# Optimization experiments

Measured on AMD Instinct MI355X. Metric: run time of the kernel, lower is better.

Reference implementation:

```python
import jax, jax.numpy as jnp
import numpy as np

G, M, H, HEADS, FFN, MAX_DIST, E = 8, 1024, 256, 8, 1024, 5, 131072
N = G * M
HD = H // HEADS

def _ln(x, g, b, eps=1e-5):
    m = x.mean(-1, keepdims=True)
    v = ((x - m) ** 2).mean(-1, keepdims=True)
    return (x - m) / jnp.sqrt(v + eps) * g + b

def _forward(x, gcn_w, gcn_b, qkv_w, qkv_b, proj_w, proj_b,
             ln1_g, ln1_b, ln2_g, ln2_b, ffn1_w, ffn1_b, ffn2_w, ffn2_b,
             bias_emb, oln1_g, oln1_b, oln2_g, oln2_b,
             offn1_w, offn1_b, offn2_w, offn2_b, edge_index, batch):
    src, dst = edge_index[0], edge_index[1]
    # --- local conv: GCNConv (self-loops + symmetric normalization) ---
    sl = jnp.arange(N, dtype=src.dtype)
    s2 = jnp.concatenate([src, sl]); d2 = jnp.concatenate([dst, sl])
    xw = x @ gcn_w.T
    deg = jax.ops.segment_sum(jnp.ones_like(d2, dtype=x.dtype), d2, num_segments=N)
    dinv = jnp.where(deg > 0, 1.0 / jnp.sqrt(deg), 0.0)
    norm = dinv[s2] * dinv[d2]
    x_local = jax.ops.segment_sum(xw[s2] * norm[:, None], d2, num_segments=N) + gcn_b
    # --- to_dense_batch ---
    counts = jax.ops.segment_sum(jnp.ones(N, jnp.int32), batch, num_segments=G)
    starts = jnp.concatenate([jnp.zeros(1, jnp.int32), jnp.cumsum(counts)[:-1]])
    local = jnp.arange(N, dtype=jnp.int32) - starts[batch]
    dense_x = jnp.zeros((G, M, H), x.dtype).at[batch, local].set(x)
    mask = jnp.zeros((G, M), bool).at[batch, local].set(True)
    # --- SPD via batched boolean adjacency powering (== per-node BFS capped at MAX_DIST) ---
    g_e = batch[src]
    valid = (batch[src] == batch[dst]) & (src != dst)
    ls, ld = local[src], local[dst]
    adj = jnp.zeros((G, M, M), bool).at[g_e, ls, ld].max(valid).at[g_e, ld, ls].max(valid)
    dist = jnp.full((G, M, M), MAX_DIST + 1, jnp.int32)
    eye = jnp.eye(M, dtype=bool)[None]
    dist = jnp.where(eye & mask[:, :, None], 0, dist)
    reach = adj
    dist = jnp.where(reach, jnp.minimum(dist, 1), dist)
    for d in range(2, MAX_DIST + 1):
        reach = jnp.einsum('gij,gjk->gik', reach.astype(x.dtype), adj.astype(x.dtype)) > 0
        dist = jnp.where(reach, jnp.minimum(dist, d), dist)
    attn_bias = bias_emb[dist][..., 0]  # [G, M, M]
    # --- Graphormer encoder layer (layers=1) ---
    h = dense_x
    qkv = (h @ qkv_w.T + qkv_b).reshape(G, M, 3, HEADS, HD).transpose(2, 0, 3, 1, 4)
    q, k, v = qkv[0], qkv[1], qkv[2]  # [G, heads, M, hd]
    scores = jnp.einsum('ghqd,ghkd->ghqk', q, k) * (HD ** -0.5)
    scores = scores + attn_bias[:, None].astype(scores.dtype)
    pad = ~mask
    scores = jnp.where(pad[:, None, None, :], -jnp.inf, scores)
    attn = jax.nn.softmax(scores, axis=-1)
    out = jnp.einsum('ghqk,ghkd->ghqd', attn, v).transpose(0, 2, 1, 3).reshape(G, M, H)
    out = out @ proj_w.T + proj_b
    h = _ln(h + out, ln1_g, ln1_b)
    ff = jax.nn.gelu(h @ ffn1_w.T + ffn1_b, approximate=False) @ ffn2_w.T + ffn2_b
    h = _ln(h + ff, ln2_g, ln2_b)
    h = jnp.where(pad[..., None], 0.0, h)
    x_global = h[batch, local]
    # --- GPS combine + outer FFN (dropout = identity at eval) ---
    y = _ln(x + (x_local + x_global), oln1_g, oln1_b)
    ff2 = jax.nn.gelu(y @ offn1_w.T + offn1_b, approximate=False) @ offn2_w.T + offn2_b
    return _ln(y + ff2, oln2_g, oln2_b)

def setup_inputs() -> dict:
    key = jax.random.key(0)
    ks = jax.random.split(key, 16)
    w = lambda k, *s: jax.random.normal(k, s, jnp.float32) * 0.02
    src = jax.random.randint(ks[0], (E,), 0, N, jnp.int32)
    # keep each edge inside one graph (graphs are contiguous blocks of M nodes)
    dst = (src // M) * M + jax.random.randint(ks[1], (E,), 0, M, jnp.int32)
    return dict(
        x=jax.random.normal(ks[2], (N, H), jnp.float32),
        gcn_w=w(ks[3], H, H), gcn_b=jnp.zeros((H,), jnp.float32),
        qkv_w=w(ks[4], 3 * H, H), qkv_b=jnp.zeros((3 * H,), jnp.float32),
        proj_w=w(ks[5], H, H), proj_b=jnp.zeros((H,), jnp.float32),
        ln1_g=jnp.ones((H,), jnp.float32), ln1_b=jnp.zeros((H,), jnp.float32),
        ln2_g=jnp.ones((H,), jnp.float32), ln2_b=jnp.zeros((H,), jnp.float32),
        ffn1_w=w(ks[6], FFN, H), ffn1_b=jnp.zeros((FFN,), jnp.float32),
        ffn2_w=w(ks[7], H, FFN), ffn2_b=jnp.zeros((H,), jnp.float32),
        bias_emb=w(ks[8], MAX_DIST + 2, 1),
        oln1_g=jnp.ones((H,), jnp.float32), oln1_b=jnp.zeros((H,), jnp.float32),
        oln2_g=jnp.ones((H,), jnp.float32), oln2_b=jnp.zeros((H,), jnp.float32),
        offn1_w=w(ks[9], FFN, H), offn1_b=jnp.zeros((FFN,), jnp.float32),
        offn2_w=w(ks[10], H, FFN), offn2_b=jnp.zeros((H,), jnp.float32),
        edge_index=jnp.stack([src, dst]),
        batch=(jnp.arange(N, dtype=jnp.int32) // M),
    )

def reference(x, gcn_w, gcn_b, qkv_w, qkv_b, proj_w, proj_b,
              ln1_g, ln1_b, ln2_g, ln2_b, ffn1_w, ffn1_b, ffn2_w, ffn2_b,
              bias_emb, oln1_g, oln1_b, oln2_g, oln2_b,
              offn1_w, offn1_b, offn2_w, offn2_b, edge_index, batch):
    return _forward(x, gcn_w, gcn_b, qkv_w, qkv_b, proj_w, proj_b,
                    ln1_g, ln1_b, ln2_g, ln2_b, ffn1_w, ffn1_b, ffn2_w, ffn2_b,
                    bias_emb, oln1_g, oln1_b, oln2_g, oln2_b,
                    offn1_w, offn1_b, offn2_w, offn2_b, edge_index, batch)
```

## Files before the change

### kernel.cpp

```cpp
#include <hip/hip_runtime.h>
#include <hip/hip_bf16.h>
#include <cstdint>

#define G 8
#define M 1024
#define H 256
#define HEADS 8
#define FFND 1024
#define NE 131072
#define NN (G*M)
#define HD 32

typedef unsigned long long u64;
typedef uint8_t u8;
typedef unsigned short ushort_t;
typedef __attribute__((ext_vector_type(8))) short bf16x8;
typedef __attribute__((ext_vector_type(4))) float f32x4;

__device__ __forceinline__ short f2b(float v) {
  __hip_bfloat16 h = __float2bfloat16(v);
  return *reinterpret_cast<short*>(&h);
}
__device__ __forceinline__ float b2f(unsigned int u) {
  union { float f; unsigned int i; } v; v.i = u << 16; return v.f;
}

typedef __attribute__((address_space(1))) const void gvoid;
typedef __attribute__((address_space(3))) void lvoid;
__device__ __forceinline__ void gload16(const void* g, void* l) {
  __builtin_amdgcn_global_load_lds((gvoid*)g, (lvoid*)l, 16, 0, 0);
}

__global__ void k_prep(const int* __restrict__ srcv, const int* __restrict__ dstv,
                       int* __restrict__ deg, int* __restrict__ deg2) {
  int e = blockIdx.x * 256 + threadIdx.x;
  if (e >= NE) return;
  int d = dstv[e], s = srcv[e];
  atomicAdd(&deg[d], 1);
  if (s != d) { atomicAdd(&deg2[s], 1); atomicAdd(&deg2[d], 1); }
}

__global__ __launch_bounds__(1024) void k_scan2(const int* __restrict__ deg, const int* __restrict__ deg2,
                                                int* __restrict__ starts, int* __restrict__ starts2,
                                                float* __restrict__ dinv) {
  __shared__ int tmp[1024];
  const int* in = blockIdx.x ? deg2 : deg;
  int* outp = blockIdx.x ? starts2 : starts;
  int t = threadIdx.x;
  int base = t * 8;
  int v[8]; int s = 0;
  #pragma unroll
  for (int i = 0; i < 8; ++i) { v[i] = in[base + i]; s += v[i]; }
  if (blockIdx.x == 0) {
    #pragma unroll
    for (int i = 0; i < 8; ++i) dinv[base + i] = rsqrtf((float)(v[i] + 1));
  }
  tmp[t] = s;
  __syncthreads();
  for (int off = 1; off < 1024; off <<= 1) {
    int x = (t >= off) ? tmp[t - off] : 0;
    __syncthreads();
    tmp[t] += x;
    __syncthreads();
  }
  int ex = (t == 0) ? 0 : tmp[t - 1];
  #pragma unroll
  for (int i = 0; i < 8; ++i) { outp[base + i] = ex; ex += v[i]; }
}

__global__ void k_fillb(const int* __restrict__ srcv, const int* __restrict__ dstv,
                        const int* __restrict__ starts, int* __restrict__ cursor,
                        int* __restrict__ csr,
                        const int* __restrict__ starts2, int* __restrict__ cur2,
                        int* __restrict__ nbr) {
  int e = blockIdx.x * 256 + threadIdx.x;
  if (e >= NE) return;
  int d = dstv[e], s = srcv[e];
  int pos = atomicAdd(&cursor[d], 1);
  csr[starts[d] + pos] = s;
  if (s != d) {
    int p = atomicAdd(&cur2[s], 1); nbr[starts2[s] + p] = d;
    p = atomicAdd(&cur2[d], 1);     nbr[starts2[d] + p] = s;
  }
}

__global__ __launch_bounds__(256) void k_gather(const int* __restrict__ csr,
    const int* __restrict__ starts, const int* __restrict__ deg,
    const float* __restrict__ dinv, const ushort_t* __restrict__ xwb,
    const float* __restrict__ gcn_b, float* __restrict__ xloc) {
  int d = blockIdx.x, t = threadIdx.x;
  int s0 = starts[d], cnt = deg[d];
  float acc = 0.f;
  for (int j = 0; j < cnt; ++j) {
    int s = csr[s0 + j];
    acc += dinv[s] * b2f(xwb[(size_t)s * H + t]);
  }
  float di = dinv[d];
  float self = b2f(xwb[(size_t)d * H + t]);
  xloc[(size_t)d * H + t] = di * acc + di * di * self + gcn_b[t];
}

__global__ __launch_bounds__(1024) void k_spdm(const int* __restrict__ starts2,
                                               const int* __restrict__ deg2,
                                               const int* __restrict__ nbr,
                                               u8* __restrict__ dist) {
  __shared__ unsigned int Abuf[1024], Bbuf[1024];
  __shared__ u8 dtile[1024][32];
  const int g = blockIdx.x >> 5, w = blockIdx.x & 31;
  const int i = threadIdx.x;
  const int gi = (g << 10) | i;
  unsigned int self = ((i >> 5) == w) ? (1u << (i & 31)) : 0u;
  Abuf[i] = self;
  uint4 six; six.x = six.y = six.z = six.w = 0x06060606u;
  *reinterpret_cast<uint4*>(&dtile[i][0])  = six;
  *reinterpret_cast<uint4*>(&dtile[i][16]) = six;
  if (self) dtile[i][i & 31] = 0;
  const int s0 = starts2[gi], cnt = deg2[gi];
  unsigned int* prev = Abuf;
  unsigned int* cur  = Bbuf;
  unsigned int vis = self;
  __syncthreads();
  for (int l = 1; l <= 5; ++l) {
    unsigned int acc = vis;
    for (int e = 0; e < cnt; ++e)
      acc |= prev[nbr[s0 + e] & 1023];
    unsigned int newly = acc & ~vis;
    while (newly) {
      int k = __ffs(newly) - 1;
      newly &= newly - 1;
      dtile[i][k] = (u8)l;
    }
    cur[i] = acc;
    vis = acc;
    __syncthreads();
    unsigned int* tsw = prev; prev = cur; cur = tsw;
  }
  u8* drow = dist + ((size_t)gi << 10) + w * 32;
  *reinterpret_cast<uint4*>(drow)      = *reinterpret_cast<const uint4*>(&dtile[i][0]);
  *reinterpret_cast<uint4*>(drow + 16) = *reinterpret_cast<const uint4*>(&dtile[i][16]);
}

#define WB_GCN   0
#define WB_QKV   65536
#define WB_PROJ  262144
#define WB_FFN1  327680
#define WB_FFN2  589824
#define WB_OFFN1 851968
#define WB_OFFN2 1114112
#define WB_TOTAL 1376256
#define NXBLK 2048
#define NWBLK 5376

__global__ void k_cvtall(const float* __restrict__ x,
                         const float* p0, const float* p1, const float* p2,
                         const float* p3, const float* p4, const float* p5, const float* p6,
                         const float* __restrict__ qkv_b,
                         ushort_t* __restrict__ x_bf, ushort_t* __restrict__ w_bf,
                         float* __restrict__ bias_cat) {
  int bid = blockIdx.x, t = threadIdx.x;
  if (bid < NXBLK) {
    int i = bid * 256 + t;
    float4 v = reinterpret_cast<const float4*>(x)[i];
    unsigned int lo = (unsigned int)(ushort_t)f2b(v.x) | ((unsigned int)(ushort_t)f2b(v.y) << 16);
    unsigned int hi = (unsigned int)(ushort_t)f2b(v.z) | ((unsigned int)(ushort_t)f2b(v.w) << 16);
    reinterpret_cast<uint2*>(x_bf)[i] = make_uint2(lo, hi);
  } else if (bid < NXBLK + NWBLK) {
    int i = (bid - NXBLK) * 256 + t;
    const float* src; int off;
    if (i < WB_QKV)        { src = p0; off = i; }
    else if (i < WB_PROJ)  { src = p1; off = i - WB_QKV; }
    else if (i < WB_FFN1)  { src = p2; off = i - WB_PROJ; }
    else if (i < WB_FFN2)  { src = p3; off = i - WB_FFN1; }
    else if (i < WB_OFFN1) { src = p4; off = i - WB_FFN2; }
    else if (i < WB_OFFN2) { src = p5; off = i - WB_OFFN1; }
    else                   { src = p6; off = i - WB_OFFN2; }
    w_bf[i] = (ushort_t)f2b(src[off]);
  } else {
    for (int i = t; i < 1024; i += 256) bias_cat[i] = (i < 256) ? 0.f : qkv_b[i - 256];
  }
}

template<int BM, int ACT, int OMODE>
__global__ __launch_bounds__(256) void k_mgemm(const short* __restrict__ A,
                                               const short* __restrict__ W,
                                               const float* __restrict__ bias,
                                               short* __restrict__ Cb,
                                               short* __restrict__ Cb2,
                                               int K, int O) {
  constexpr int FM = BM / 32;
  __shared__ __attribute__((aligned(16))) short As[BM * 64];
  __shared__ __attribute__((aligned(16))) short Ws[64 * 64];
  const int tid = threadIdx.x;
  const int lane = tid & 63, wbase = tid & 192;
  const int wid = tid >> 6;
  const int lg = lane >> 4, lr = lane & 15;
  const int wm = wid >> 1, wn = wid & 1;
  const int m0 = blockIdx.y * BM, n0 = blockIdx.x * 64;
  f32x4 acc[FM][2];
  #pragma unroll
  for (int i = 0; i < FM; ++i)
    #pragma unroll
    for (int j = 0; j < 2; ++j)
      acc[i][j] = (f32x4){0.f, 0.f, 0.f, 0.f};

  for (int k0 = 0; k0 < K; k0 += 64) {
    #pragma unroll
    for (int c = 0; c < BM / 32; ++c) {
      int chunk = c * 256 + tid;
      int row = chunk >> 3, ks = chunk & 7;
      int srcks = ks ^ (row & 7);
      gload16(A + (size_t)(m0 + row) * K + k0 + srcks * 8,
              (char*)As + (c * 256 + wbase) * 16);
    }
    #pragma unroll
    for (int c = 0; c < 2; ++c) {
      int chunk = c * 256 + tid;
      int row = chunk >> 3, ks = chunk & 7;
      int srcks = ks ^ (row & 7);
      gload16(W + (size_t)(n0 + row) * K + k0 + srcks * 8,
              (char*)Ws + (c * 256 + wbase) * 16);
    }
    __syncthreads();
    #pragma unroll
    for (int kk = 0; kk < 2; ++kk) {
      const int d = kk * 4 + lg;
      bf16x8 b[2];
      #pragma unroll
      for (int fn = 0; fn < 2; ++fn) {
        int r = wn * 32 + fn * 16 + lr;
        b[fn] = *reinterpret_cast<const bf16x8*>((const char*)Ws + r * 128 + ((d ^ (r & 7)) * 16));
      }
      #pragma unroll
      for (int fm = 0; fm < FM; ++fm) {
        int r = wm * (BM / 2) + fm * 16 + lr;
        bf16x8 a = *reinterpret_cast<const bf16x8*>((const char*)As + r * 128 + ((d ^ (r & 7)) * 16));
        acc[fm][0] = __builtin_amdgcn_mfma_f32_16x16x32_bf16(a, b[0], acc[fm][0], 0, 0, 0);
        acc[fm][1] = __builtin_amdgcn_mfma_f32_16x16x32_bf16(a, b[1], acc[fm][1], 0, 0, 0);
      }
    }
    __syncthreads();
  }
  #pragma unroll
  for (int fm = 0; fm < FM; ++fm)
    #pragma unroll
    for (int fn = 0; fn < 2; ++fn)
      #pragma unroll
      for (int rg = 0; rg < 4; ++rg) {
        int r = m0 + wm * (BM / 2) + fm * 16 + lg * 4 + rg;
        int cc = n0 + wn * 32 + fn * 16 + lr;
        float v = acc[fm][fn][rg] + (bias ? bias[cc] : 0.f);
        if (ACT == 1) v = 0.5f * v * (1.0f + erff(v * 0.70710678118654752f));
        if (OMODE == 1) Cb[(size_t)r * O + cc] = f2b(v);
        else {
          if (cc < 256) Cb2[(size_t)r * 256 + cc] = f2b(v);
          else          Cb[(size_t)r * 768 + cc - 256] = f2b(v);
        }
      }
}

template<int KK, int OUTB>
__global__ __launch_bounds__(256) void k_gemmln(const short* __restrict__ A,
                                                const short* __restrict__ W,
                                                const float* __restrict__ bias,
                                                const float* __restrict__ res1,
                                                const float* __restrict__ gam,
                                                const float* __restrict__ bet,
                                                float* __restrict__ outf,
                                                ushort_t* __restrict__ outb) {
  __shared__ __attribute__((aligned(16))) short As[32 * 64];
  __shared__ __attribute__((aligned(16))) short Ws[256 * 64];
  __shared__ float redS[4][32], redQ[4][32];
  const int tid = threadIdx.x, lane = tid & 63, wid = tid >> 6;
  const int wbase = tid & 192;
  const int lg = lane >> 4, lr = lane & 15;
  const int m0 = blockIdx.x * 32;
  f32x4 acc[2][4];
  #pragma unroll
  for (int i = 0; i < 2; ++i)
    #pragma unroll
    for (int j = 0; j < 4; ++j)
      acc[i][j] = (f32x4){0.f, 0.f, 0.f, 0.f};

  for (int k0 = 0; k0 < KK; k0 += 64) {
    {
      int row = tid >> 3, ks = tid & 7, srcks = ks ^ (row & 7);
      gload16(A + (size_t)(m0 + row) * KK + k0 + srcks * 8,
              (char*)As + wbase * 16);
    }
    #pragma unroll
    for (int c = 0; c < 8; ++c) {
      int chunk = c * 256 + tid;
      int row = chunk >> 3, ks = chunk & 7;
      int srcks = ks ^ (row & 7);
      gload16(W + (size_t)row * KK + k0 + srcks * 8,
              (char*)Ws + (c * 256 + wbase) * 16);
    }
    __syncthreads();
    #pragma unroll
    for (int kk = 0; kk < 2; ++kk) {
      const int d = kk * 4 + lg;
      bf16x8 a[2];
      #pragma unroll
      for (int fr = 0; fr < 2; ++fr) {
        int r = fr * 16 + lr;
        a[fr] = *reinterpret_cast<const bf16x8*>((const char*)As + r * 128 + ((d ^ (r & 7)) * 16));
      }
      #pragma unroll
      for (int fc = 0; fc < 4; ++fc) {
        int r = wid * 64 + fc * 16 + lr;
        bf16x8 b = *reinterpret_cast<const bf16x8*>((const char*)Ws + r * 128 + ((d ^ (r & 7)) * 16));
        acc[0][fc] = __builtin_amdgcn_mfma_f32_16x16x32_bf16(a[0], b, acc[0][fc], 0, 0, 0);
        acc[1][fc] = __builtin_amdgcn_mfma_f32_16x16x32_bf16(a[1], b, acc[1][fc], 0, 0, 0);
      }
    }
    __syncthreads();
  }

  float vs[2][4][4];
  float ps[2][4], pq[2][4];
  #pragma unroll
  for (int fr = 0; fr < 2; ++fr)
    #pragma unroll
    for (int rg = 0; rg < 4; ++rg) { ps[fr][rg] = 0.f; pq[fr][rg] = 0.f; }
  #pragma unroll
  for (int fc = 0; fc < 4; ++fc) {
    int col = wid * 64 + fc * 16 + lr;
    float bv = bias[col];
    #pragma unroll
    for (int fr = 0; fr < 2; ++fr)
      #pragma unroll
      for (int rg = 0; rg < 4; ++rg) {
        int row = m0 + fr * 16 + 4 * lg + rg;
        float v = acc[fr][fc][rg] + bv + res1[(size_t)row * 256 + col];
        vs[fr][fc][rg] = v;
        ps[fr][rg] += v; pq[fr][rg] += v * v;
      }
  }
  #pragma unroll
  for (int fr = 0; fr < 2; ++fr)
    #pragma unroll
    for (int rg = 0; rg < 4; ++rg) {
      float s = ps[fr][rg], q = pq[fr][rg];
      s += __shfl_xor(s, 1); q += __shfl_xor(q, 1);
      s += __shfl_xor(s, 2); q += __shfl_xor(q, 2);
      s += __shfl_xor(s, 4); q += __shfl_xor(q, 4);
      s += __shfl_xor(s, 8); q += __shfl_xor(q, 8);
      ps[fr][rg] = s; pq[fr][rg] = q;
    }
  if (lr == 0) {
    #pragma unroll
    for (int fr = 0; fr < 2; ++fr)
      #pragma unroll
      for (int rg = 0; rg < 4; ++rg) {
        redS[wid][fr * 16 + 4 * lg + rg] = ps[fr][rg];
        redQ[wid][fr * 16 + 4 * lg + rg] = pq[fr][rg];
      }
  }
  __syncthreads();
  #pragma unroll
  for (int fr = 0; fr < 2; ++fr)
    #pragma unroll
    for (int rg = 0; rg < 4; ++rg) {
      int rl = fr * 16 + 4 * lg + rg;
      float S = redS[0][rl] + redS[1][rl] + redS[2][rl] + redS[3][rl];
      float Q = redQ[0][rl] + redQ[1][rl] + redQ[2][rl] + redQ[3][rl];
      float mean = S * (1.0f / 256.0f);
      float rstd = rsqrtf(Q * (1.0f / 256.0f) - mean * mean + 1e-5f);
      #pragma unroll
      for (int fc = 0; fc < 4; ++fc) {
        int col = wid * 64 + fc * 16 + lr;
        float v = (vs[fr][fc][rg] - mean) * rstd * gam[col] + bet[col];
        size_t o = (size_t)(m0 + rl) * 256 + col;
        outf[o] = v;
        if (OUTB) outb[o] = (ushort_t)f2b(v);
      }
    }
}

__global__ __launch_bounds__(256) void k_attn(const ushort_t* __restrict__ qkv,
                                              const u8* __restrict__ dist,
                                              const float* __restrict__ emb,
                                              short* __restrict__ attno) {
  __shared__ __attribute__((aligned(16))) char KsB[32 * 128];
  __shared__ __attribute__((aligned(16))) char VtB[32 * 128 + 64];
  __shared__ __attribute__((aligned(16))) char PB[4][16 * 128];
  __shared__ __attribute__((aligned(16))) u8 Ds[32 * 128];
  __shared__ float semb[8];
  const int g = blockIdx.z, head = blockIdx.y;
  const int q0 = blockIdx.x * 64;
  const int t = threadIdx.x, lane = t & 63, wid = t >> 6;
  const int lg = lane >> 4, lr = lane & 15;
  if (t < 7) semb[t] = emb[t] * 1.44269504088896341f;
  const size_t nodebase = (size_t)(g * M) * 768;
  const float C1 = 0.17677669529663687f * 1.44269504088896341f;

  bf16x8 qfrag = *reinterpret_cast<const bf16x8*>(
      qkv + nodebase + (size_t)(q0 + wid * 16 + lr) * 768 + head * 32 + lg * 8);

  const int srow = t >> 2, sc = t & 3;
  const int prow8 = t >> 3, pslot = (t & 7) ^ (prow8 & 7);
  uint4 kr, vr, dr;
  {
    size_t kn = nodebase + (size_t)(srow) * 768 + head * 32;
    kr = *reinterpret_cast<const uint4*>(qkv + kn + 256 + sc * 8);
    vr = *reinterpret_cast<const uint4*>(qkv + kn + 512 + sc * 8);
    dr = *reinterpret_cast<const uint4*>(dist + (size_t)(g * M + srow) * M + q0 + sc * 16);
  }

  f32x4 o0 = {0.f, 0.f, 0.f, 0.f}, o1 = {0.f, 0.f, 0.f, 0.f};
  float lpart[4] = {0.f, 0.f, 0.f, 0.f};
  char* pb = PB[wid];
  const int kp = srow >> 1;
  const int odd = srow & 1;
  const int d0 = sc * 8;
  int r8f[4], slK[4], slD[4];
  #pragma unroll
  for (int fn = 0; fn < 4; ++fn) {
    r8f[fn] = fn * 8 + (lr >> 1);
    slK[fn] = (((lr & 1) << 2) | lg) ^ (r8f[fn] & 7);
    slD[fn] = (((lr & 1) << 2) | wid) ^ (r8f[fn] & 7);
  }

  for (int kt = 0; kt < 16; ++kt) {
    *reinterpret_cast<uint4*>(KsB + prow8 * 128 + pslot * 16) = kr;
    *reinterpret_cast<uint4*>(Ds + prow8 * 128 + pslot * 16) = dr;
    {
      uint4 pvr;
      pvr.x = (unsigned int)__shfl_xor((int)vr.x, 4);
      pvr.y = (unsigned int)__shfl_xor((int)vr.y, 4);
      pvr.z = (unsigned int)__shfl_xor((int)vr.z, 4);
      pvr.w = (unsigned int)__shfl_xor((int)vr.w, 4);
      unsigned int ev[4], ov[4];
      ev[0] = odd ? pvr.x : vr.x; ev[1] = odd ? pvr.y : vr.y;
      ev[2] = odd ? pvr.z : vr.z; ev[3] = odd ? pvr.w : vr.w;
      ov[0] = odd ? vr.x : pvr.x; ov[1] = odd ? vr.y : pvr.y;
      ov[2] = odd ? vr.z : pvr.z; ov[3] = odd ? vr.w : pvr.w;
      #pragma unroll
      for (int di = 0; di < 4; ++di) {
        int dd = odd * 4 + di;
        int d = d0 + dd;
        unsigned int e16 = (dd & 1) ? (ev[dd >> 1] >> 16) : (ev[dd >> 1] & 0xffff);
        unsigned int o16 = (dd & 1) ? (ov[dd >> 1] >> 16) : (ov[dd >> 1] & 0xffff);
        *reinterpret_cast<unsigned int*>(VtB + d * 128 + ((d >> 3) << 4) + ((kp << 2) ^ ((d & 7) << 4)))
            = e16 | (o16 << 16);
      }
    }
    __syncthreads();

    {
      int ktn = (kt + 1) & 15;
      size_t kn = nodebase + (size_t)(ktn * 64 + srow) * 768 + head * 32;
      kr = *reinterpret_cast<const uint4*>(qkv + kn + 256 + sc * 8);
      vr = *reinterpret_cast<const uint4*>(qkv + kn + 512 + sc * 8);
      dr = *reinterpret_cast<const uint4*>(dist + (size_t)(g * M + ktn * 64 + srow) * M + q0 + sc * 16);
    }

    f32x4 s[4];
    unsigned int d4[4];
    #pragma unroll
    for (int fn = 0; fn < 4; ++fn) {
      bf16x8 b = *reinterpret_cast<const bf16x8*>(KsB + r8f[fn] * 128 + slK[fn] * 16);
      s[fn] = __builtin_amdgcn_mfma_f32_16x16x32_bf16(qfrag, b, (f32x4){0.f,0.f,0.f,0.f}, 0, 0, 0);
      d4[fn] = *reinterpret_cast<const unsigned int*>(Ds + r8f[fn] * 128 + slD[fn] * 16 + 4 * lg);
    }
    #pragma unroll
    for (int fn = 0; fn < 4; ++fn)
      #pragma unroll
      for (int rg = 0; rg < 4; ++rg)
        s[fn][rg] = exp2f(s[fn][rg] * C1 + semb[(d4[fn] >> (8 * rg)) & 255]);
    #pragma unroll
    for (int rg = 0; rg < 4; ++rg)
      lpart[rg] += (s[0][rg] + s[1][rg]) + (s[2][rg] + s[3][rg]);

    #pragma unroll
    for (int fn = 0; fn < 4; ++fn)
      #pragma unroll
      for (int rg = 0; rg < 4; ++rg) {
        int qq = 4 * lg + rg, key = fn * 16 + lr;
        *reinterpret_cast<ushort_t*>(pb + qq * 128 + ((key * 2) ^ ((qq & 7) << 4))) =
            (ushort_t)f2b(s[fn][rg]);
      }

    #pragma unroll
    for (int kh = 0; kh < 2; ++kh) {
      int c = kh * 4 + lg;
      int chx = (c << 4) ^ ((lr & 7) << 4);
      bf16x8 a  = *reinterpret_cast<const bf16x8*>(pb + lr * 128 + chx);
      bf16x8 b0 = *reinterpret_cast<const bf16x8*>(VtB + lr * 128 + ((lr >> 3) << 4) + chx);
      bf16x8 b1 = *reinterpret_cast<const bf16x8*>(VtB + (16 + lr) * 128 + (((16 + lr) >> 3) << 4) + chx);
      o0 = __builtin_amdgcn_mfma_f32_16x16x32_bf16(a, b0, o0, 0, 0, 0);
      o1 = __builtin_amdgcn_mfma_f32_16x16x32_bf16(a, b1, o1, 0, 0, 0);
    }
    __syncthreads();
  }

  #pragma unroll
  for (int rg = 0; rg < 4; ++rg) {
    float l = lpart[rg];
    l += __shfl_xor(l, 1);
    l += __shfl_xor(l, 2);
    l += __shfl_xor(l, 4);
    l += __shfl_xor(l, 8);
    float inv = 1.0f / l;
    size_t qn = (size_t)(g * M + q0 + wid * 16 + 4 * lg + rg);
    attno[qn * H + head * 32 + lr]      = f2b(o0[rg] * inv);
    attno[qn * H + head * 32 + 16 + lr] = f2b(o1[rg] * inv);
  }
}

__global__ __launch_bounds__(256) void k_ln(const float* __restrict__ a, const float* __restrict__ b,
                                            const float* __restrict__ c3,
                                            const float* __restrict__ gam, const float* __restrict__ bet,
                                            float* __restrict__ out, ushort_t* __restrict__ outb) {
  int wid = threadIdx.x >> 6, lane = threadIdx.x & 63;
  int row = blockIdx.x * 4 + wid;
  size_t base = (size_t)row * H + lane * 4;
  float4 v = *reinterpret_cast<const float4*>(a + base);
  float4 vb = *reinterpret_cast<const float4*>(b + base);
  v.x += vb.x; v.y += vb.y; v.z += vb.z; v.w += vb.w;
  if (c3) {
    float4 vc = *reinterpret_cast<const float4*>(c3 + base);
    v.x += vc.x; v.y += vc.y; v.z += vc.z; v.w += vc.w;
  }
  float s = v.x + v.y + v.z + v.w;
  float s2 = v.x*v.x + v.y*v.y + v.z*v.z + v.w*v.w;
  #pragma unroll
  for (int off = 1; off <= 32; off <<= 1) {
    s  += __shfl_xor(s, off);
    s2 += __shfl_xor(s2, off);
  }
  float mean = s * (1.0f / 256.0f);
  float rstd = rsqrtf(s2 * (1.0f / 256.0f) - mean * mean + 1e-5f);
  float4 gg = *reinterpret_cast<const float4*>(gam + lane * 4);
  float4 bb = *reinterpret_cast<const float4*>(bet + lane * 4);
  float4 r;
  r.x = (v.x - mean) * rstd * gg.x + bb.x;
  r.y = (v.y - mean) * rstd * gg.y + bb.y;
  r.z = (v.z - mean) * rstd * gg.z + bb.z;
  r.w = (v.w - mean) * rstd * gg.w + bb.w;
  *reinterpret_cast<float4*>(out + base) = r;
  if (outb) {
    unsigned int lo = (unsigned int)(ushort_t)f2b(r.x) | ((unsigned int)(ushort_t)f2b(r.y) << 16);
    unsigned int hi = (unsigned int)(ushort_t)f2b(r.z) | ((unsigned int)(ushort_t)f2b(r.w) << 16);
    *reinterpret_cast<uint2*>(outb + base) = make_uint2(lo, hi);
  }
}

extern "C" void kernel_launch(void* const* d_in, const int* in_sizes, int n_in,
                              void* d_out, int out_size, void* d_ws, size_t ws_size,
                              hipStream_t stream) {
  const float* x      = (const float*)d_in[0];
  const float* gcn_w  = (const float*)d_in[1];
  const float* gcn_b  = (const float*)d_in[2];
  const float* qkv_w  = (const float*)d_in[3];
  const float* qkv_b  = (const float*)d_in[4];
  const float* proj_w = (const float*)d_in[5];
  const float* proj_b = (const float*)d_in[6];
  const float* ln1_g  = (const float*)d_in[7];
  const float* ln1_b  = (const float*)d_in[8];
  const float* ln2_g  = (const float*)d_in[9];
  const float* ln2_b  = (const float*)d_in[10];
  const float* ffn1_w = (const float*)d_in[11];
  const float* ffn1_b = (const float*)d_in[12];
  const float* ffn2_w = (const float*)d_in[13];
  const float* ffn2_b = (const float*)d_in[14];
  const float* bias_e = (const float*)d_in[15];
  const float* oln1_g = (const float*)d_in[16];
  const float* oln1_b = (const float*)d_in[17];
  const float* oln2_g = (const float*)d_in[18];
  const float* oln2_b = (const float*)d_in[19];
  const float* offn1_w= (const float*)d_in[20];
  const float* offn1_b= (const float*)d_in[21];
  const float* offn2_w= (const float*)d_in[22];
  const float* offn2_b= (const float*)d_in[23];
  const int*   eidx   = (const int*)d_in[24];
  const int* esrc = eidx;
  const int* edst = eidx + NE;

  char* wsp = (char*)d_ws;
  size_t off = 0;
  auto alloc = [&](size_t bytes) { void* p = wsp + off; off += (bytes + 255) & ~255ull; return p; };
  const size_t SZ_NH = (size_t)NN * H * 4;
  ushort_t* x_bf  = (ushort_t*)alloc((size_t)NN * H * 2);
  ushort_t* w_bf  = (ushort_t*)alloc((size_t)WB_TOTAL * 2);
  float* bias_cat = (float*)alloc(1024 * 4);
  ushort_t* xwb   = (ushort_t*)alloc((size_t)NN * H * 2);
  float* xloc = (float*)alloc(SZ_NH);
  float* dinv = (float*)alloc((size_t)NN * 4);
  int*   deg  = (int*)  alloc((size_t)NN * 4);
  int* cursor = (int*)  alloc((size_t)NN * 4);
  int*  deg2  = (int*)  alloc((size_t)NN * 4);
  int* cursor2= (int*)  alloc((size_t)NN * 4);
  int* starts = (int*)  alloc((size_t)NN * 4);
  int* starts2= (int*)  alloc((size_t)NN * 4);
  int*   csr  = (int*)  alloc((size_t)NE * 4);
  int*   nbr  = (int*)  alloc((size_t)2 * NE * 4);
  u8*    dist = (u8*)   alloc((size_t)NN * M);
  ushort_t* qkvb = (ushort_t*)alloc((size_t)NN * 768 * 2);
  float* h1   = (float*)alloc(SZ_NH);
  ushort_t* h1_bf = (ushort_t*)alloc((size_t)NN * H * 2);
  float* h2   = (float*)alloc(SZ_NH);
  float* y    = (float*)alloc(SZ_NH);

  ushort_t* attno = x_bf;
  ushort_t* mid = (ushort_t*)dist;
  ushort_t* y_bf = h1_bf;
  float* outp = (float*)d_out;

  ushort_t* proj_wb = w_bf + WB_PROJ;
  ushort_t* ffn1_wb = w_bf + WB_FFN1;
  ushort_t* ffn2_wb = w_bf + WB_FFN2;
  ushort_t* offn1_wb= w_bf + WB_OFFN1;
  ushort_t* offn2_wb= w_bf + WB_OFFN2;

  hipMemsetAsync(deg, 0, (size_t)4 * NN * 4, stream);

  k_cvtall<<<NXBLK + NWBLK + 1, 256, 0, stream>>>(x, gcn_w, qkv_w, proj_w, ffn1_w,
                                                  ffn2_w, offn1_w, offn2_w, qkv_b,
                                                  x_bf, w_bf, bias_cat);

  k_prep<<<NE / 256, 256, 0, stream>>>(esrc, edst, deg, deg2);
  k_scan2<<<2, 1024, 0, stream>>>(deg, deg2, starts, starts2, dinv);
  k_fillb<<<NE / 256, 256, 0, stream>>>(esrc, edst, starts, cursor, csr, starts2, cursor2, nbr);

  k_mgemm<128, 0, 2><<<dim3(1024 / 64, NN / 128), 256, 0, stream>>>(
      (const short*)x_bf, (const short*)w_bf, bias_cat, (short*)qkvb, (short*)xwb, 256, 1024);
  k_gather<<<NN, 256, 0, stream>>>(csr, starts, deg, dinv, xwb, gcn_b, xloc);

  k_spdm<<<G * 32, 1024, 0, stream>>>(starts2, deg2, nbr, dist);

  k_attn<<<dim3(M / 64, HEADS, G), 256, 0, stream>>>(qkvb, dist, bias_e, (short*)attno);
  k_gemmln<256, 1><<<NN / 32, 256, 0, stream>>>(
      (const short*)attno, (const short*)proj_wb, proj_b, x, ln1_g, ln1_b, h1, h1_bf);
  k_mgemm<128, 1, 1><<<dim3(FFND / 64, NN / 128), 256, 0, stream>>>(
      (const short*)h1_bf, (const short*)ffn1_wb, ffn1_b, (short*)mid, nullptr, 256, FFND);
  k_gemmln<1024, 0><<<NN / 32, 256, 0, stream>>>(
      (const short*)mid, (const short*)ffn2_wb, ffn2_b, h1, ln2_g, ln2_b, h2, nullptr);

  k_ln<<<NN / 4, 256, 0, stream>>>(x, xloc, h2, oln1_g, oln1_b, y, y_bf);
  k_mgemm<128, 1, 1><<<dim3(FFND / 64, NN / 128), 256, 0, stream>>>(
      (const short*)y_bf, (const short*)offn1_wb, offn1_b, (short*)mid, nullptr, 256, FFND);
  k_gemmln<1024, 0><<<NN / 32, 256, 0, stream>>>(
      (const short*)mid, (const short*)offn2_wb, offn2_b, y, oln2_g, oln2_b, outp, nullptr);
}
```

Baseline: 374.6 us.

## Split attention keys across blocks, split-K gemmln, fuse outer LayerNorm

Attention now splits the key range into two halves handled by separate blocks. Each block writes unnormalized partial outputs and row sums, and a new combine kernel merges them into the bf16 attention output. The GEMM+LayerNorm kernel doubles to 512 threads, with two thread groups each doing half of the K reduction; partials are summed through shared memory. The FFN2 GEMM+LN also fuses the outer residual LayerNorm, which removes the separate k_ln kernel and the h2 buffer. Together these aim to raise parallelism and cut launches, at the cost of extra fp32 partial traffic and a combine pass.

```diff
diff --git a/kernel.cpp b/kernel.cpp
--- a/kernel.cpp
+++ b/kernel.cpp
@@ -258,20 +258,25 @@
       }
 }
 
-template<int KK, int OUTB>
-__global__ __launch_bounds__(256) void k_gemmln(const short* __restrict__ A,
+template<int KK, int OUTB, int LN2>
+__global__ __launch_bounds__(512) void k_gemmln(const short* __restrict__ A,
                                                 const short* __restrict__ W,
                                                 const float* __restrict__ bias,
                                                 const float* __restrict__ res1,
                                                 const float* __restrict__ gam,
                                                 const float* __restrict__ bet,
+                                                const float* __restrict__ res2a,
+                                                const float* __restrict__ res2b,
+                                                const float* __restrict__ gam2,
+                                                const float* __restrict__ bet2,
                                                 float* __restrict__ outf,
                                                 ushort_t* __restrict__ outb) {
-  __shared__ __attribute__((aligned(16))) short As[32 * 64];
-  __shared__ __attribute__((aligned(16))) short Ws[256 * 64];
+  __shared__ __attribute__((aligned(16))) short As[2][32 * 64];
+  __shared__ __attribute__((aligned(16))) short Ws[2][256 * 64];
   __shared__ float redS[4][32], redQ[4][32];
-  const int tid = threadIdx.x, lane = tid & 63, wid = tid >> 6;
-  const int wbase = tid & 192;
+  const int tid = threadIdx.x, lane = tid & 63;
+  const int hg = tid >> 8, ht = tid & 255;
+  const int cw = (tid >> 6) & 3;
   const int lg = lane >> 4, lr = lane & 15;
   const int m0 = blockIdx.x * 32;
   f32x4 acc[2][4];
@@ -281,19 +286,20 @@
     for (int j = 0; j < 4; ++j)
       acc[i][j] = (f32x4){0.f, 0.f, 0.f, 0.f};
 
-  for (int k0 = 0; k0 < KK; k0 += 64) {
+  for (int st = 0; st < KK / 128; ++st) {
+    const int k0 = hg * (KK / 2) + st * 64;
     {
-      int row = tid >> 3, ks = tid & 7, srcks = ks ^ (row & 7);
+      int row = ht >> 3, ks = ht & 7, srcks = ks ^ (row & 7);
       gload16(A + (size_t)(m0 + row) * KK + k0 + srcks * 8,
-              (char*)As + wbase * 16);
+              (char*)As[hg] + (ht & 192) * 16);
     }
     #pragma unroll
     for (int c = 0; c < 8; ++c) {
-      int chunk = c * 256 + tid;
+      int chunk = c * 256 + ht;
       int row = chunk >> 3, ks = chunk & 7;
       int srcks = ks ^ (row & 7);
       gload16(W + (size_t)row * KK + k0 + srcks * 8,
-              (char*)Ws + (c * 256 + wbase) * 16);
+              (char*)Ws[hg] + (c * 256 + (ht & 192)) * 16);
     }
     __syncthreads();
     #pragma unroll
@@ -303,12 +309,12 @@
       #pragma unroll
       for (int fr = 0; fr < 2; ++fr) {
         int r = fr * 16 + lr;
-        a[fr] = *reinterpret_cast<const bf16x8*>((const char*)As + r * 128 + ((d ^ (r & 7)) * 16));
+        a[fr] = *reinterpret_cast<const bf16x8*>((const char*)As[hg] + r * 128 + ((d ^ (r & 7)) * 16));
       }
       #pragma unroll
       for (int fc = 0; fc < 4; ++fc) {
-        int r = wid * 64 + fc * 16 + lr;
-        bf16x8 b = *reinterpret_cast<const bf16x8*>((const char*)Ws + r * 128 + ((d ^ (r & 7)) * 16));
+        int r = cw * 64 + fc * 16 + lr;
+        bf16x8 b = *reinterpret_cast<const bf16x8*>((const char*)Ws[hg] + r * 128 + ((d ^ (r & 7)) * 16));
         acc[0][fc] = __builtin_amdgcn_mfma_f32_16x16x32_bf16(a[0], b, acc[0][fc], 0, 0, 0);
         acc[1][fc] = __builtin_amdgcn_mfma_f32_16x16x32_bf16(a[1], b, acc[1][fc], 0, 0, 0);
       }
@@ -316,78 +322,162 @@
     __syncthreads();
   }
 
+  float* xch = reinterpret_cast<float*>(&Ws[0][0]);
+  if (hg == 1) {
+    float* p = xch + ht * 33;
+    #pragma unroll
+    for (int fr = 0; fr < 2; ++fr)
+      #pragma unroll
+      for (int fc = 0; fc < 4; ++fc)
+        #pragma unroll
+        for (int rg = 0; rg < 4; ++rg)
+          p[(fr * 4 + fc) * 4 + rg] = acc[fr][fc][rg];
+  }
+  __syncthreads();
+
   float vs[2][4][4];
-  float ps[2][4], pq[2][4];
-  #pragma unroll
-  for (int fr = 0; fr < 2; ++fr)
-    #pragma unroll
-    for (int rg = 0; rg < 4; ++rg) { ps[fr][rg] = 0.f; pq[fr][rg] = 0.f; }
-  #pragma unroll
-  for (int fc = 0; fc < 4; ++fc) {
-    int col = wid * 64 + fc * 16 + lr;
-    float bv = bias[col];
+  float mean1[2][4], rstd1[2][4];
+  if (hg == 0) {
+    float* p = xch + ht * 33;
+    float ps[2][4], pq[2][4];
     #pragma unroll
     for (int fr = 0; fr < 2; ++fr)
       #pragma unroll
+      for (int rg = 0; rg < 4; ++rg) { ps[fr][rg] = 0.f; pq[fr][rg] = 0.f; }
+    #pragma unroll
+    for (int fc = 0; fc < 4; ++fc) {
+      int col = cw * 64 + fc * 16 + lr;
+      float bv = bias[col];
+      #pragma unroll
+      for (int fr = 0; fr < 2; ++fr)
+        #pragma unroll
+        for (int rg = 0; rg < 4; ++rg) {
+          int row = m0 + fr * 16 + 4 * lg + rg;
+          float v = acc[fr][fc][rg] + p[(fr * 4 + fc) * 4 + rg] + bv
+                  + res1[(size_t)row * 256 + col];
+          vs[fr][fc][rg] = v;
+          ps[fr][rg] += v; pq[fr][rg] += v * v;
+        }
+    }
+    #pragma unroll
+    for (int fr = 0; fr < 2; ++fr)
+      #pragma unroll
       for (int rg = 0; rg < 4; ++rg) {
-        int row = m0 + fr * 16 + 4 * lg + rg;
-        float v = acc[fr][fc][rg] + bv + res1[(size_t)row * 256 + col];
-        vs[fr][fc][rg] = v;
-        ps[fr][rg] += v; pq[fr][rg] += v * v;
-      }
-  }
-  #pragma unroll
-  for (int fr = 0; fr < 2; ++fr)
-    #pragma unroll
-    for (int rg = 0; rg < 4; ++rg) {
-      float s = ps[fr][rg], q = pq[fr][rg];
-      s += __shfl_xor(s, 1); q += __shfl_xor(q, 1);
-      s += __shfl_xor(s, 2); q += __shfl_xor(q, 2);
-      s += __shfl_xor(s, 4); q += __shfl_xor(q, 4);
-      s += __shfl_xor(s, 8); q += __shfl_xor(q, 8);
-      ps[fr][rg] = s; pq[fr][rg] = q;
-    }
-  if (lr == 0) {
+        float s = ps[fr][rg], q = pq[fr][rg];
+        s += __shfl_xor(s, 1); q += __shfl_xor(q, 1);
+        s += __shfl_xor(s, 2); q += __shfl_xor(q, 2);
+        s += __shfl_xor(s, 4); q += __shfl_xor(q, 4);
+        s += __shfl_xor(s, 8); q += __shfl_xor(q, 8);
+        if (lr == 0) {
+          redS[cw][fr * 16 + 4 * lg + rg] = s;
+          redQ[cw][fr * 16 + 4 * lg + rg] = q;
+        }
+      }
+  }
+  __syncthreads();
+  if (hg == 0) {
     #pragma unroll
     for (int fr = 0; fr < 2; ++fr)
       #pragma unroll
       for (int rg = 0; rg < 4; ++rg) {
-        redS[wid][fr * 16 + 4 * lg + rg] = ps[fr][rg];
-        redQ[wid][fr * 16 + 4 * lg + rg] = pq[fr][rg];
-      }
-  }
-  __syncthreads();
-  #pragma unroll
-  for (int fr = 0; fr < 2; ++fr)
-    #pragma unroll
-    for (int rg = 0; rg < 4; ++rg) {
-      int rl = fr * 16 + 4 * lg + rg;
-      float S = redS[0][rl] + redS[1][rl] + redS[2][rl] + redS[3][rl];
-      float Q = redQ[0][rl] + redQ[1][rl] + redQ[2][rl] + redQ[3][rl];
-      float mean = S * (1.0f / 256.0f);
-      float rstd = rsqrtf(Q * (1.0f / 256.0f) - mean * mean + 1e-5f);
+        int rl = fr * 16 + 4 * lg + rg;
+        float S = redS[0][rl] + redS[1][rl] + redS[2][rl] + redS[3][rl];
+        float Q = redQ[0][rl] + redQ[1][rl] + redQ[2][rl] + redQ[3][rl];
+        float mn = S * (1.0f / 256.0f);
+        mean1[fr][rg] = mn;
+        rstd1[fr][rg] = rsqrtf(Q * (1.0f / 256.0f) - mn * mn + 1e-5f);
+      }
+  }
+
+  if (LN2) {
+    __syncthreads();
+    if (hg == 0) {
+      float ps[2][4], pq[2][4];
+      #pragma unroll
+      for (int fr = 0; fr < 2; ++fr)
+        #pragma unroll
+        for (int rg = 0; rg < 4; ++rg) { ps[fr][rg] = 0.f; pq[fr][rg] = 0.f; }
       #pragma unroll
       for (int fc = 0; fc < 4; ++fc) {
-        int col = wid * 64 + fc * 16 + lr;
-        float v = (vs[fr][fc][rg] - mean) * rstd * gam[col] + bet[col];
-        size_t o = (size_t)(m0 + rl) * 256 + col;
-        outf[o] = v;
-        if (OUTB) outb[o] = (ushort_t)f2b(v);
-      }
-    }
+        int col = cw * 64 + fc * 16 + lr;
+        float g1 = gam[col], b1 = bet[col];
+        #pragma unroll
+        for (int fr = 0; fr < 2; ++fr)
+          #pragma unroll
+          for (int rg = 0; rg < 4; ++rg) {
+            int row = m0 + fr * 16 + 4 * lg + rg;
+            float v1n = (vs[fr][fc][rg] - mean1[fr][rg]) * rstd1[fr][rg] * g1 + b1;
+            float v = v1n + res2a[(size_t)row * 256 + col] + res2b[(size_t)row * 256 + col];
+            vs[fr][fc][rg] = v;
+            ps[fr][rg] += v; pq[fr][rg] += v * v;
+          }
+      }
+      #pragma unroll
+      for (int fr = 0; fr < 2; ++fr)
+        #pragma unroll
+        for (int rg = 0; rg < 4; ++rg) {
+          float s = ps[fr][rg], q = pq[fr][rg];
+          s += __shfl_xor(s, 1); q += __shfl_xor(q, 1);
+          s += __shfl_xor(s, 2); q += __shfl_xor(q, 2);
+          s += __shfl_xor(s, 4); q += __shfl_xor(q, 4);
+          s += __shfl_xor(s, 8); q += __shfl_xor(q, 8);
+          if (lr == 0) {
+            redS[cw][fr * 16 + 4 * lg + rg] = s;
+            redQ[cw][fr * 16 + 4 * lg + rg] = q;
+          }
+        }
+    }
+    __syncthreads();
+    if (hg == 0) {
+      #pragma unroll
+      for (int fr = 0; fr < 2; ++fr)
+        #pragma unroll
+        for (int rg = 0; rg < 4; ++rg) {
+          int rl = fr * 16 + 4 * lg + rg;
+          float S = redS[0][rl] + redS[1][rl] + redS[2][rl] + redS[3][rl];
+          float Q = redQ[0][rl] + redQ[1][rl] + redQ[2][rl] + redQ[3][rl];
+          float mn = S * (1.0f / 256.0f);
+          mean1[fr][rg] = mn;
+          rstd1[fr][rg] = rsqrtf(Q * (1.0f / 256.0f) - mn * mn + 1e-5f);
+        }
+    }
+  }
+
+  if (hg == 0) {
+    const float* gma = LN2 ? gam2 : gam;
+    const float* bta = LN2 ? bet2 : bet;
+    #pragma unroll
+    for (int fr = 0; fr < 2; ++fr)
+      #pragma unroll
+      for (int rg = 0; rg < 4; ++rg) {
+        int rl = fr * 16 + 4 * lg + rg;
+        #pragma unroll
+        for (int fc = 0; fc < 4; ++fc) {
+          int col = cw * 64 + fc * 16 + lr;
+          float v = (vs[fr][fc][rg] - mean1[fr][rg]) * rstd1[fr][rg] * gma[col] + bta[col];
+          size_t o = (size_t)(m0 + rl) * 256 + col;
+          outf[o] = v;
+          if (OUTB) outb[o] = (ushort_t)f2b(v);
+        }
+      }
+  }
 }
 
 __global__ __launch_bounds__(256) void k_attn(const ushort_t* __restrict__ qkv,
                                               const u8* __restrict__ dist,
                                               const float* __restrict__ emb,
-                                              short* __restrict__ attno) {
+                                              float* __restrict__ po0,
+                                              float* __restrict__ po1,
+                                              float* __restrict__ pl) {
   __shared__ __attribute__((aligned(16))) char KsB[32 * 128];
   __shared__ __attribute__((aligned(16))) char VtB[32 * 128 + 64];
   __shared__ __attribute__((aligned(16))) char PB[4][16 * 128];
   __shared__ __attribute__((aligned(16))) u8 Ds[32 * 128];
   __shared__ float semb[8];
   const int g = blockIdx.z, head = blockIdx.y;
-  const int q0 = blockIdx.x * 64;
+  const int sp = blockIdx.x >> 4, qblk = blockIdx.x & 15;
+  const int q0 = qblk * 64;
+  const int kt0 = sp * 8;
   const int t = threadIdx.x, lane = t & 63, wid = t >> 6;
   const int lg = lane >> 4, lr = lane & 15;
   if (t < 7) semb[t] = emb[t] * 1.44269504088896341f;
@@ -401,10 +491,10 @@
   const int prow8 = t >> 3, pslot = (t & 7) ^ (prow8 & 7);
   uint4 kr, vr, dr;
   {
-    size_t kn = nodebase + (size_t)(srow) * 768 + head * 32;
+    size_t kn = nodebase + (size_t)(kt0 * 64 + srow) * 768 + head * 32;
     kr = *reinterpret_cast<const uint4*>(qkv + kn + 256 + sc * 8);
     vr = *reinterpret_cast<const uint4*>(qkv + kn + 512 + sc * 8);
-    dr = *reinterpret_cast<const uint4*>(dist + (size_t)(g * M + srow) * M + q0 + sc * 16);
+    dr = *reinterpret_cast<const uint4*>(dist + (size_t)(g * M + kt0 * 64 + srow) * M + q0 + sc * 16);
   }
 
   f32x4 o0 = {0.f, 0.f, 0.f, 0.f}, o1 = {0.f, 0.f, 0.f, 0.f};
@@ -421,7 +511,7 @@
     slD[fn] = (((lr & 1) << 2) | wid) ^ (r8f[fn] & 7);
   }
 
-  for (int kt = 0; kt < 16; ++kt) {
+  for (int kt = kt0; kt < kt0 + 8; ++kt) {
     *reinterpret_cast<uint4*>(KsB + prow8 * 128 + pslot * 16) = kr;
     *reinterpret_cast<uint4*>(Ds + prow8 * 128 + pslot * 16) = dr;
     {
@@ -494,6 +584,7 @@
     __syncthreads();
   }
 
+  float* po = sp ? po1 : po0;
   #pragma unroll
   for (int rg = 0; rg < 4; ++rg) {
     float l = lpart[rg];
@@ -501,49 +592,34 @@
     l += __shfl_xor(l, 2);
     l += __shfl_xor(l, 4);
     l += __shfl_xor(l, 8);
-    float inv = 1.0f / l;
-    size_t qn = (size_t)(g * M + q0 + wid * 16 + 4 * lg + rg);
-    attno[qn * H + head * 32 + lr]      = f2b(o0[rg] * inv);
-    attno[qn * H + head * 32 + 16 + lr] = f2b(o1[rg] * inv);
-  }
-}
-
-__global__ __launch_bounds__(256) void k_ln(const float* __restrict__ a, const float* __restrict__ b,
-                                            const float* __restrict__ c3,
-                                            const float* __restrict__ gam, const float* __restrict__ bet,
-                                            float* __restrict__ out, ushort_t* __restrict__ outb) {
-  int wid = threadIdx.x >> 6, lane = threadIdx.x & 63;
-  int row = blockIdx.x * 4 + wid;
-  size_t base = (size_t)row * H + lane * 4;
-  float4 v = *reinterpret_cast<const float4*>(a + base);
-  float4 vb = *reinterpret_cast<const float4*>(b + base);
-  v.x += vb.x; v.y += vb.y; v.z += vb.z; v.w += vb.w;
-  if (c3) {
-    float4 vc = *reinterpret_cast<const float4*>(c3 + base);
-    v.x += vc.x; v.y += vc.y; v.z += vc.z; v.w += vc.w;
-  }
-  float s = v.x + v.y + v.z + v.w;
-  float s2 = v.x*v.x + v.y*v.y + v.z*v.z + v.w*v.w;
-  #pragma unroll
-  for (int off = 1; off <= 32; off <<= 1) {
-    s  += __shfl_xor(s, off);
-    s2 += __shfl_xor(s2, off);
-  }
-  float mean = s * (1.0f / 256.0f);
-  float rstd = rsqrtf(s2 * (1.0f / 256.0f) - mean * mean + 1e-5f);
-  float4 gg = *reinterpret_cast<const float4*>(gam + lane * 4);
-  float4 bb = *reinterpret_cast<const float4*>(bet + lane * 4);
-  float4 r;
-  r.x = (v.x - mean) * rstd * gg.x + bb.x;
-  r.y = (v.y - mean) * rstd * gg.y + bb.y;
-  r.z = (v.z - mean) * rstd * gg.z + bb.z;
-  r.w = (v.w - mean) * rstd * gg.w + bb.w;
-  *reinterpret_cast<float4*>(out + base) = r;
-  if (outb) {
-    unsigned int lo = (unsigned int)(ushort_t)f2b(r.x) | ((unsigned int)(ushort_t)f2b(r.y) << 16);
-    unsigned int hi = (unsigned int)(ushort_t)f2b(r.z) | ((unsigned int)(ushort_t)f2b(r.w) << 16);
-    *reinterpret_cast<uint2*>(outb + base) = make_uint2(lo, hi);
-  }
+    int q = q0 + wid * 16 + 4 * lg + rg;
+    size_t qn = (size_t)(g * M + q);
+    po[qn * H + head * 32 + lr]      = o0[rg];
+    po[qn * H + head * 32 + 16 + lr] = o1[rg];
+    if (lr == 0)
+      pl[(sp << 16) + ((g * HEADS + head) << 10) + q] = l;
+  }
+}
+
+__global__ __launch_bounds__(256) void k_acomb(const float* __restrict__ po0,
+                                               const float* __restrict__ po1,
+                                               const float* __restrict__ pl,
+                                               ushort_t* __restrict__ attno) {
+  int i4 = blockIdx.x * 256 + threadIdx.x;
+  int idx = i4 * 4;
+  int q = idx >> 8;
+  int col = idx & 255;
+  int head = col >> 5;
+  int g = q >> 10, ql = q & 1023;
+  int li = ((g * HEADS + head) << 10) + ql;
+  float inv = 1.0f / (pl[li] + pl[65536 + li]);
+  float4 a = reinterpret_cast<const float4*>(po0)[i4];
+  float4 b = reinterpret_cast<const float4*>(po1)[i4];
+  unsigned int lo = (unsigned int)(ushort_t)f2b((a.x + b.x) * inv)
+                  | ((unsigned int)(ushort_t)f2b((a.y + b.y) * inv) << 16);
+  unsigned int hi = (unsigned int)(ushort_t)f2b((a.z + b.z) * inv)
+                  | ((unsigned int)(ushort_t)f2b((a.w + b.w) * inv) << 16);
+  reinterpret_cast<uint2*>(attno)[i4] = make_uint2(lo, hi);
 }
 
 extern "C" void kernel_launch(void* const* d_in, const int* in_sizes, int n_in,
@@ -599,12 +675,14 @@
   ushort_t* qkvb = (ushort_t*)alloc((size_t)NN * 768 * 2);
   float* h1   = (float*)alloc(SZ_NH);
   ushort_t* h1_bf = (ushort_t*)alloc((size_t)NN * H * 2);
-  float* h2   = (float*)alloc(SZ_NH);
   float* y    = (float*)alloc(SZ_NH);
+  float* pl   = (float*)alloc((size_t)2 * 65536 * 4);
 
   ushort_t* attno = x_bf;
   ushort_t* mid = (ushort_t*)dist;
   ushort_t* y_bf = h1_bf;
+  float* po0 = h1;
+  float* po1 = y;
   float* outp = (float*)d_out;
 
   ushort_t* proj_wb = w_bf + WB_PROJ;
@@ -629,17 +707,20 @@
 
   k_spdm<<<G * 32, 1024, 0, stream>>>(starts2, deg2, nbr, dist);
 
-  k_attn<<<dim3(M / 64, HEADS, G), 256, 0, stream>>>(qkvb, dist, bias_e, (short*)attno);
-  k_gemmln<256, 1><<<NN / 32, 256, 0, stream>>>(
-      (const short*)attno, (const short*)proj_wb, proj_b, x, ln1_g, ln1_b, h1, h1_bf);
+  k_attn<<<dim3(32, HEADS, G), 256, 0, stream>>>(qkvb, dist, bias_e, po0, po1, pl);
+  k_acomb<<<NN * H / 4 / 256, 256, 0, stream>>>(po0, po1, pl, attno);
+
+  k_gemmln<256, 1, 0><<<NN / 32, 512, 0, stream>>>(
+      (const short*)attno, (const short*)proj_wb, proj_b, x, ln1_g, ln1_b,
+      nullptr, nullptr, nullptr, nullptr, h1, h1_bf);
   k_mgemm<128, 1, 1><<<dim3(FFND / 64, NN / 128), 256, 0, stream>>>(
       (const short*)h1_bf, (const short*)ffn1_wb, ffn1_b, (short*)mid, nullptr, 256, FFND);
-  k_gemmln<1024, 0><<<NN / 32, 256, 0, stream>>>(
-      (const short*)mid, (const short*)ffn2_wb, ffn2_b, h1, ln2_g, ln2_b, h2, nullptr);
-
-  k_ln<<<NN / 4, 256, 0, stream>>>(x, xloc, h2, oln1_g, oln1_b, y, y_bf);
+  k_gemmln<1024, 1, 1><<<NN / 32, 512, 0, stream>>>(
+      (const short*)mid, (const short*)ffn2_wb, ffn2_b, h1, ln2_g, ln2_b,
+      x, xloc, oln1_g, oln1_b, y, y_bf);
   k_mgemm<128, 1, 1><<<dim3(FFND / 64, NN / 128), 256, 0, stream>>>(
       (const short*)y_bf, (const short*)offn1_wb, offn1_b, (short*)mid, nullptr, 256, FFND);
-  k_gemmln<1024, 0><<<NN / 32, 256, 0, stream>>>(
-      (const short*)mid, (const short*)offn2_wb, offn2_b, y, oln2_g, oln2_b, outp, nullptr);
-}
+  k_gemmln<1024, 0, 0><<<NN / 32, 512, 0, stream>>>(
+      (const short*)mid, (const short*)offn2_wb, offn2_b, y, oln2_g, oln2_b,
+      nullptr, nullptr, nullptr, nullptr, outp, nullptr);
+}
```

New measurement: 361.2 us. -3.6%, faster.
